# Kernel tuning notes

Measured on AMD Instinct MI355X. Metric: run time of the kernel, lower is better.

## Reference

```python
import jax, jax.numpy as jnp
import numpy as np

CH = 64
CF = CH // 8  # f/g projection channels


def setup_inputs() -> dict:
    key = jax.random.key(0)
    k1, k2, k3, k4, k5 = jax.random.split(key, 5)
    x = jax.random.normal(k1, (8, 64, 64, CH), dtype=jnp.float32)
    kernel_f = 0.02 * jax.random.normal(k2, (1, 1, CH, CF), dtype=jnp.float32)
    kernel_g = 0.02 * jax.random.normal(k3, (1, 1, CH, CF), dtype=jnp.float32)
    kernel_h = 0.02 * jax.random.normal(k4, (1, 1, CH, CH), dtype=jnp.float32)
    gamma = 0.02 * jax.random.normal(k5, (1,), dtype=jnp.float32)
    return {"x": x, "kernel_f": kernel_f, "kernel_g": kernel_g,
            "kernel_h": kernel_h, "gamma": gamma}


def reference(x, kernel_f, kernel_g, kernel_h, gamma):
    B, H, W, C = x.shape
    N = H * W
    xf = x.reshape(B, N, C)  # flatten spatial; 1x1 conv == matmul over channels
    f = jnp.einsum('bnc,cd->bnd', xf, kernel_f[0, 0])  # [B,N,CF]
    g = jnp.einsum('bnc,cd->bnd', xf, kernel_g[0, 0])  # [B,N,CF]
    h = jnp.einsum('bnc,cd->bnd', xf, kernel_h[0, 0])  # [B,N,C]
    s = jnp.einsum('bnd,bmd->bnm', g, f)  # g @ f^T, [B,N,N]
    beta = jax.nn.softmax(s, axis=-1)
    o = jnp.einsum('bnm,bmc->bnc', beta, h)  # [B,N,C]
    out = gamma * o.reshape(B, H, W, C) + x
    return out
```

## Files before the change

kernel.cpp:

```cpp
#include <hip/hip_runtime.h>
#include <hip/hip_bf16.h>

typedef __attribute__((ext_vector_type(4)))  float f32x4;
typedef __attribute__((ext_vector_type(16))) float f32x16;
typedef __attribute__((ext_vector_type(8)))  short bf16x8;

#define LOG2E 1.44269504088896340736f

#if __has_builtin(__builtin_amdgcn_exp2f)
static __device__ __forceinline__ float exp2_native(float x) {
  return __builtin_amdgcn_exp2f(x);
}
#else
extern "C" __device__ float __ocml_native_exp2_f32(float);
static __device__ __forceinline__ float exp2_native(float x) {
  return __ocml_native_exp2_f32(x);
}
#endif

static __device__ __forceinline__ unsigned int pack_trunc_f(float a, float b) {
  return __builtin_amdgcn_perm(__float_as_uint(b), __float_as_uint(a), 0x07060302);
}

typedef const __attribute__((address_space(1))) unsigned int gu32;
typedef __attribute__((address_space(3))) unsigned int lu32;
static __device__ __forceinline__ void gload_lds16(const void* g, void* l) {
  __builtin_amdgcn_global_load_lds((gu32*)g, (lu32*)l, 16, 0, 0);
}

__global__ __launch_bounds__(256) void proj_kernel(
    const float* __restrict__ x, const float* __restrict__ kf,
    const float* __restrict__ kg, const float* __restrict__ kh,
    unsigned short* __restrict__ f_b, unsigned short* __restrict__ g_b,
    unsigned short* __restrict__ h_p)
{
  __shared__ unsigned short Kt[80*72];
  const int t = threadIdx.x, blk = blockIdx.x;

  #pragma unroll
  for (int r = 0; r < 20; ++r) {
    int idx = r*256 + t;
    int o = idx >> 6, c = idx & 63;
    float v = (o < 8) ? kf[c*8 + o]
            : (o < 16) ? kg[c*8 + (o-8)] * LOG2E
            : kh[c*64 + (o-16)];
    Kt[o*72 + c] = (unsigned short)(__float_as_uint(v) >> 16);
  }
  __syncthreads();

  const int w = t >> 6, lane = t & 63, l15 = lane & 15, quad = lane >> 4;
  const int Rbase = blk*64 + w*16;
  const int R = Rbase + l15;

  bf16x8 af[2];
  #pragma unroll
  for (int kk = 0; kk < 2; ++kk) {
    const float* xp = x + (long)R*64 + kk*32 + quad*8;
    float4 v0 = *(const float4*)xp;
    float4 v1 = *(const float4*)(xp + 4);
    union { unsigned int u[4]; bf16x8 v; } p;
    p.u[0] = pack_trunc_f(v0.x, v0.y);
    p.u[1] = pack_trunc_f(v0.z, v0.w);
    p.u[2] = pack_trunc_f(v1.x, v1.y);
    p.u[3] = pack_trunc_f(v1.z, v1.w);
    af[kk] = p.v;
  }

  f32x4 acc[5];
  #pragma unroll
  for (int nt = 0; nt < 5; ++nt) { f32x4 z = {}; acc[nt] = z; }

  #pragma unroll
  for (int nt = 0; nt < 5; ++nt)
    #pragma unroll
    for (int kk = 0; kk < 2; ++kk) {
      bf16x8 bfv = *(const bf16x8*)&Kt[(nt*16 + l15)*72 + kk*32 + quad*8];
      acc[nt] = __builtin_amdgcn_mfma_f32_16x16x32_bf16(af[kk], bfv, acc[nt], 0, 0, 0);
    }

  const int bt = Rbase >> 12;
  const int kt = (Rbase >> 7) & 31;
  const int base = ((blk & 1) << 6) + (w << 4);
  const int pi = base + ((quad & 1) << 3) + (((quad >> 1) & 1) << 2);

  #pragma unroll
  for (int rr = 0; rr < 4; ++rr) {
    const int nq = (Rbase + quad*4 + rr) & 4095;
    unsigned short v = (unsigned short)(__float_as_uint(acc[0][rr]) >> 16);
    if (l15 < 8) f_b[((long)bt*4096 + nq)*8 + l15] = v;
    else         g_b[((long)bt*4096 + nq)*8 + (l15 - 8)] = v;
  }
  #pragma unroll
  for (int nt = 1; nt < 5; ++nt) {
    const int c = (nt - 1)*16 + l15;
    uint2 v;
    v.x = pack_trunc_f(acc[nt][0], acc[nt][1]);
    v.y = pack_trunc_f(acc[nt][2], acc[nt][3]);
    *(uint2*)(h_p + ((long)(bt*32 + kt)*64 + c)*136 + pi) = v;
  }
}

__global__ __launch_bounds__(256, 4) void attn_kernel(
    const unsigned short* __restrict__ f_b, const unsigned short* __restrict__ g_b,
    const unsigned short* __restrict__ h_p, unsigned short* __restrict__ po,
    float* __restrict__ pl)
{
  __shared__ unsigned short bufs[2][9728];

  const int t = threadIdx.x;
  const int w = t >> 6, lane = t & 63, l31 = lane & 31, a = lane >> 5;
  const int qb = blockIdx.x, b = blockIdx.y, sp = blockIdx.z;
  const int q0w = qb*128 + w*32;

  bf16x8 gfv;
  {
    bf16x8 gv = *(const bf16x8*)(g_b + ((long)b*4096 + q0w + l31)*8);
    bf16x8 z = {};
    gfv = (a == 0) ? gv : z;
  }

  f32x16 oacc[2];
  { f32x16 z = {}; oacc[0] = z; oacc[1] = z; }
  float l_run = 0.f;

  const char* hp_b = (const char*)h_p + (long)b*32*17408;
  const char* fb_b = (const char*)f_b + (long)b*4096*16;

  auto stage = [&](int bi, int kt) {
    const char* hsrc = hp_b + (long)kt*17408;
    const char* fsrc = fb_b + (long)kt*2048;
    char* dst = (char*)&bufs[bi][0];
    #pragma unroll
    for (int i = 0; i < 5; ++i) {
      const int off = i*4096 + w*1024;
      if (off < 19456) {
        const char* src = (off < 17408) ? (hsrc + off) : (fsrc + (off - 17408));
        gload_lds16(src + lane*16, dst + off);
      }
    }
  };

  stage(0, sp*8);

  for (int ktl = 0; ktl < 8; ++ktl) {
    __syncthreads();
    if (ktl < 7) stage((ktl + 1) & 1, sp*8 + ktl + 1);

    const unsigned short* hts = &bufs[ktl & 1][0];
    const unsigned short* fts = &bufs[ktl & 1][8704];

    #pragma unroll
    for (int mt = 0; mt < 4; ++mt) {
      bf16x8 afv = *(const bf16x8*)&fts[(mt*32 + l31)*8];
      f32x16 zz = {};
      f32x16 sc = __builtin_amdgcn_mfma_f32_32x32x16_bf16(afv, gfv, zz, 0, 0, 0);

      #pragma unroll
      for (int half = 0; half < 2; ++half) {
        const int s = mt*2 + half;
        bf16x8 bh0 = *(const bf16x8*)&hts[(l31)*136      + s*16 + a*8];
        bf16x8 bh1 = *(const bf16x8*)&hts[(32 + l31)*136 + s*16 + a*8];
        union { unsigned int u[4]; bf16x8 v; } ap;
        #pragma unroll
        for (int j = 0; j < 4; ++j) {
          float ea = exp2_native(sc[half*8 + 2*j]);
          float eb = exp2_native(sc[half*8 + 2*j + 1]);
          l_run += ea;
          l_run += eb;
          ap.u[j] = pack_trunc_f(ea, eb);
        }
        oacc[0] = __builtin_amdgcn_mfma_f32_32x32x16_bf16(ap.v, bh0, oacc[0], 0, 0, 0);
        oacc[1] = __builtin_amdgcn_mfma_f32_32x32x16_bf16(ap.v, bh1, oacc[1], 0, 0, 0);
      }
    }
  }

  const long sb = (long)sp*8 + b;
  float l = l_run + __shfl_xor(l_run, 32);
  if (lane < 32) pl[(sb << 12) + q0w + l31] = l;
  unsigned short* pob = po + ((sb << 12) + q0w)*64;
  #pragma unroll
  for (int nt = 0; nt < 2; ++nt)
    #pragma unroll
    for (int r = 0; r < 16; ++r) {
      const int q = (r & 3) + 8*(r >> 2) + 4*a;
      pob[(long)q*64 + nt*32 + l31] =
          (unsigned short)(__float_as_uint(oacc[nt][r]) >> 16);
    }
}

__global__ __launch_bounds__(256) void combine_kernel(
    const float* __restrict__ x, const unsigned short* __restrict__ po,
    const float* __restrict__ pl, const float* __restrict__ gamma_p,
    float* __restrict__ out)
{
  const long tid = (long)blockIdx.x*256 + threadIdx.x;
  const long bn = tid >> 3;
  const int c0 = (int)(tid & 7)*8;

  float l = 0.f;
  float o[8];
  #pragma unroll
  for (int i = 0; i < 8; ++i) o[i] = 0.f;
  #pragma unroll
  for (int s = 0; s < 4; ++s) {
    l += pl[(long)s*32768 + bn];
    uint4 v = *(const uint4*)(po + ((long)s*32768 + bn)*64 + c0);
    const unsigned short* pv = (const unsigned short*)&v;
    #pragma unroll
    for (int i = 0; i < 8; ++i)
      o[i] += __uint_as_float((unsigned int)pv[i] << 16);
  }
  const float scale = gamma_p[0] / l;
  const float* xp = x + bn*64 + c0;
  float4 x0 = *(const float4*)xp;
  float4 x1 = *(const float4*)(xp + 4);
  float4 r0, r1;
  r0.x = fmaf(scale, o[0], x0.x);
  r0.y = fmaf(scale, o[1], x0.y);
  r0.z = fmaf(scale, o[2], x0.z);
  r0.w = fmaf(scale, o[3], x0.w);
  r1.x = fmaf(scale, o[4], x1.x);
  r1.y = fmaf(scale, o[5], x1.y);
  r1.z = fmaf(scale, o[6], x1.z);
  r1.w = fmaf(scale, o[7], x1.w);
  float* op = out + bn*64 + c0;
  *(float4*)op = r0;
  *(float4*)(op + 4) = r1;
}

extern "C" void kernel_launch(void* const* d_in, const int* in_sizes, int n_in,
                              void* d_out, int out_size, void* d_ws, size_t ws_size,
                              hipStream_t stream) {
  const float* x  = (const float*)d_in[0];
  const float* kf = (const float*)d_in[1];
  const float* kg = (const float*)d_in[2];
  const float* kh = (const float*)d_in[3];
  const float* gamma = (const float*)d_in[4];
  float* out = (float*)d_out;

  char* ws = (char*)d_ws;
  unsigned short* h_p = (unsigned short*)ws;
  unsigned short* f_b = (unsigned short*)(ws + 4456448);
  unsigned short* g_b = (unsigned short*)(ws + 4980736);
  unsigned short* po  = (unsigned short*)(ws + 5505024);
  float*          pl  = (float*)(ws + 22282240);

  proj_kernel<<<512, 256, 0, stream>>>(x, kf, kg, kh, f_b, g_b, h_p);
  attn_kernel<<<dim3(32, 8, 4), 256, 0, stream>>>(f_b, g_b, h_p, po, pl);
  combine_kernel<<<1024, 256, 0, stream>>>(x, po, pl, gamma, out);
}
```

Before: 104.3 us.

## Fuse split-K combine into attention kernel via last-block atomic counter

Drops the separate combine kernel. Each attention block now bumps a per-(query-tile, batch) atomic counter after writing its partial outputs. The last of the four split blocks to arrive reduces the partials and writes gamma*o + x. The counters are zeroed by block 0 of the projection kernel. This saves one kernel launch and its tail. The cost is a threadfence, an atomic per block and extra register pressure for the 32-element accumulator on the finishing blocks.

Result: slower. 238.2 us (+128.3%).

```diff
diff --git a/kernel.cpp b/kernel.cpp
--- a/kernel.cpp
+++ b/kernel.cpp
@@ -32,10 +32,12 @@
     const float* __restrict__ x, const float* __restrict__ kf,
     const float* __restrict__ kg, const float* __restrict__ kh,
     unsigned short* __restrict__ f_b, unsigned short* __restrict__ g_b,
-    unsigned short* __restrict__ h_p)
+    unsigned short* __restrict__ h_p, int* __restrict__ cnt)
 {
   __shared__ unsigned short Kt[80*72];
   const int t = threadIdx.x, blk = blockIdx.x;
+
+  if (blk == 0) cnt[t] = 0;
 
   #pragma unroll
   for (int r = 0; r < 20; ++r) {
@@ -103,9 +105,12 @@
 __global__ __launch_bounds__(256, 4) void attn_kernel(
     const unsigned short* __restrict__ f_b, const unsigned short* __restrict__ g_b,
     const unsigned short* __restrict__ h_p, unsigned short* __restrict__ po,
-    float* __restrict__ pl)
+    float* __restrict__ pl, int* __restrict__ cnt,
+    const float* __restrict__ x, const float* __restrict__ gamma_p,
+    float* __restrict__ out)
 {
   __shared__ unsigned short bufs[2][9728];
+  __shared__ int sflag;
 
   const int t = threadIdx.x;
   const int w = t >> 6, lane = t & 63, l31 = lane & 31, a = lane >> 5;
@@ -187,46 +192,49 @@
       pob[(long)q*64 + nt*32 + l31] =
           (unsigned short)(__float_as_uint(oacc[nt][r]) >> 16);
     }
-}
-
-__global__ __launch_bounds__(256) void combine_kernel(
-    const float* __restrict__ x, const unsigned short* __restrict__ po,
-    const float* __restrict__ pl, const float* __restrict__ gamma_p,
-    float* __restrict__ out)
-{
-  const long tid = (long)blockIdx.x*256 + threadIdx.x;
-  const long bn = tid >> 3;
-  const int c0 = (int)(tid & 7)*8;
-
-  float l = 0.f;
-  float o[8];
-  #pragma unroll
-  for (int i = 0; i < 8; ++i) o[i] = 0.f;
+
+  __threadfence();
+  if (t == 0) {
+    int old = atomicAdd(&cnt[qb*8 + b], 1);
+    sflag = (old == 3);
+  }
+  __syncthreads();
+  if (!sflag) return;
+  __threadfence();
+
+  const int q = qb*128 + (t >> 1);
+  const int c0 = (t & 1) * 32;
+  float lsum = 0.f;
+  float o[32];
+  #pragma unroll
+  for (int i = 0; i < 32; ++i) o[i] = 0.f;
   #pragma unroll
   for (int s = 0; s < 4; ++s) {
-    l += pl[(long)s*32768 + bn];
-    uint4 v = *(const uint4*)(po + ((long)s*32768 + bn)*64 + c0);
-    const unsigned short* pv = (const unsigned short*)&v;
-    #pragma unroll
-    for (int i = 0; i < 8; ++i)
-      o[i] += __uint_as_float((unsigned int)pv[i] << 16);
-  }
-  const float scale = gamma_p[0] / l;
-  const float* xp = x + bn*64 + c0;
-  float4 x0 = *(const float4*)xp;
-  float4 x1 = *(const float4*)(xp + 4);
-  float4 r0, r1;
-  r0.x = fmaf(scale, o[0], x0.x);
-  r0.y = fmaf(scale, o[1], x0.y);
-  r0.z = fmaf(scale, o[2], x0.z);
-  r0.w = fmaf(scale, o[3], x0.w);
-  r1.x = fmaf(scale, o[4], x1.x);
-  r1.y = fmaf(scale, o[5], x1.y);
-  r1.z = fmaf(scale, o[6], x1.z);
-  r1.w = fmaf(scale, o[7], x1.w);
-  float* op = out + bn*64 + c0;
-  *(float4*)op = r0;
-  *(float4*)(op + 4) = r1;
+    const long sbb = (long)s*8 + b;
+    lsum += pl[(sbb << 12) + q];
+    const unsigned short* ps = po + ((sbb << 12) + q)*64 + c0;
+    #pragma unroll
+    for (int v4 = 0; v4 < 4; ++v4) {
+      uint4 v = *(const uint4*)(ps + v4*8);
+      const unsigned short* pv = (const unsigned short*)&v;
+      #pragma unroll
+      for (int i = 0; i < 8; ++i)
+        o[v4*8 + i] += __uint_as_float((unsigned int)pv[i] << 16);
+    }
+  }
+  const float scale = gamma_p[0] / lsum;
+  const float* xp = x + ((long)b*4096 + q)*64 + c0;
+  float* op = out + ((long)b*4096 + q)*64 + c0;
+  #pragma unroll
+  for (int v4 = 0; v4 < 8; ++v4) {
+    float4 xv = *(const float4*)(xp + v4*4);
+    float4 r;
+    r.x = fmaf(scale, o[v4*4 + 0], xv.x);
+    r.y = fmaf(scale, o[v4*4 + 1], xv.y);
+    r.z = fmaf(scale, o[v4*4 + 2], xv.z);
+    r.w = fmaf(scale, o[v4*4 + 3], xv.w);
+    *(float4*)(op + v4*4) = r;
+  }
 }
 
 extern "C" void kernel_launch(void* const* d_in, const int* in_sizes, int n_in,
@@ -245,8 +253,9 @@
   unsigned short* g_b = (unsigned short*)(ws + 4980736);
   unsigned short* po  = (unsigned short*)(ws + 5505024);
   float*          pl  = (float*)(ws + 22282240);
-
-  proj_kernel<<<512, 256, 0, stream>>>(x, kf, kg, kh, f_b, g_b, h_p);
-  attn_kernel<<<dim3(32, 8, 4), 256, 0, stream>>>(f_b, g_b, h_p, po, pl);
-  combine_kernel<<<1024, 256, 0, stream>>>(x, po, pl, gamma, out);
-}
+  int*            cnt = (int*)(ws + 22806528);
+
+  proj_kernel<<<512, 256, 0, stream>>>(x, kf, kg, kh, f_b, g_b, h_p, cnt);
+  attn_kernel<<<dim3(32, 8, 4), 256, 0, stream>>>(f_b, g_b, h_p, po, pl, cnt,
+                                                  x, gamma, out);
+}
```

## Drop split-K over keys and fuse the combine epilogue into attention

Applied to the files above, without the earlier changes.

Each attention block now iterates over all key tiles instead of a quarter of them. It applies the gamma/l scaling and residual add directly, which removes the partial-output buffers and the separate combine kernel. This saves a launch and the write and read of the bf16 partial results. The trade-off is a grid four times smaller with longer blocks, which lowers per-CU parallelism and latency hiding.

Result: slower. 116.1 us (+11.3%).

```diff
diff --git a/kernel.cpp b/kernel.cpp
--- a/kernel.cpp
+++ b/kernel.cpp
@@ -100,16 +100,17 @@
   }
 }
 
-__global__ __launch_bounds__(256, 4) void attn_kernel(
+__global__ __launch_bounds__(256) void attn_kernel(
     const unsigned short* __restrict__ f_b, const unsigned short* __restrict__ g_b,
-    const unsigned short* __restrict__ h_p, unsigned short* __restrict__ po,
-    float* __restrict__ pl)
+    const unsigned short* __restrict__ h_p,
+    const float* __restrict__ x, const float* __restrict__ gamma_p,
+    float* __restrict__ out)
 {
   __shared__ unsigned short bufs[2][9728];
 
   const int t = threadIdx.x;
   const int w = t >> 6, lane = t & 63, l31 = lane & 31, a = lane >> 5;
-  const int qb = blockIdx.x, b = blockIdx.y, sp = blockIdx.z;
+  const int qb = blockIdx.x, b = blockIdx.y;
   const int q0w = qb*128 + w*32;
 
   bf16x8 gfv;
@@ -140,11 +141,11 @@
     }
   };
 
-  stage(0, sp*8);
-
-  for (int ktl = 0; ktl < 8; ++ktl) {
+  stage(0, 0);
+
+  for (int ktl = 0; ktl < 32; ++ktl) {
     __syncthreads();
-    if (ktl < 7) stage((ktl + 1) & 1, sp*8 + ktl + 1);
+    if (ktl < 31) stage((ktl + 1) & 1, ktl + 1);
 
     const unsigned short* hts = &bufs[ktl & 1][0];
     const unsigned short* fts = &bufs[ktl & 1][8704];
@@ -175,58 +176,22 @@
     }
   }
 
-  const long sb = (long)sp*8 + b;
-  float l = l_run + __shfl_xor(l_run, 32);
-  if (lane < 32) pl[(sb << 12) + q0w + l31] = l;
-  unsigned short* pob = po + ((sb << 12) + q0w)*64;
-  #pragma unroll
-  for (int nt = 0; nt < 2; ++nt)
-    #pragma unroll
-    for (int r = 0; r < 16; ++r) {
-      const int q = (r & 3) + 8*(r >> 2) + 4*a;
-      pob[(long)q*64 + nt*32 + l31] =
-          (unsigned short)(__float_as_uint(oacc[nt][r]) >> 16);
-    }
-}
-
-__global__ __launch_bounds__(256) void combine_kernel(
-    const float* __restrict__ x, const unsigned short* __restrict__ po,
-    const float* __restrict__ pl, const float* __restrict__ gamma_p,
-    float* __restrict__ out)
-{
-  const long tid = (long)blockIdx.x*256 + threadIdx.x;
-  const long bn = tid >> 3;
-  const int c0 = (int)(tid & 7)*8;
-
-  float l = 0.f;
-  float o[8];
-  #pragma unroll
-  for (int i = 0; i < 8; ++i) o[i] = 0.f;
-  #pragma unroll
-  for (int s = 0; s < 4; ++s) {
-    l += pl[(long)s*32768 + bn];
-    uint4 v = *(const uint4*)(po + ((long)s*32768 + bn)*64 + c0);
-    const unsigned short* pv = (const unsigned short*)&v;
-    #pragma unroll
-    for (int i = 0; i < 8; ++i)
-      o[i] += __uint_as_float((unsigned int)pv[i] << 16);
-  }
-  const float scale = gamma_p[0] / l;
-  const float* xp = x + bn*64 + c0;
-  float4 x0 = *(const float4*)xp;
-  float4 x1 = *(const float4*)(xp + 4);
-  float4 r0, r1;
-  r0.x = fmaf(scale, o[0], x0.x);
-  r0.y = fmaf(scale, o[1], x0.y);
-  r0.z = fmaf(scale, o[2], x0.z);
-  r0.w = fmaf(scale, o[3], x0.w);
-  r1.x = fmaf(scale, o[4], x1.x);
-  r1.y = fmaf(scale, o[5], x1.y);
-  r1.z = fmaf(scale, o[6], x1.z);
-  r1.w = fmaf(scale, o[7], x1.w);
-  float* op = out + bn*64 + c0;
-  *(float4*)op = r0;
-  *(float4*)(op + 4) = r1;
+  const float l = l_run + __shfl_xor(l_run, 32);
+  const float gamma = gamma_p[0];
+  const float* xb = x + ((long)b*4096 + q0w)*64;
+  float* ob = out + ((long)b*4096 + q0w)*64;
+
+  #pragma unroll
+  for (int r = 0; r < 16; ++r) {
+    const int q = (r & 3) + 8*(r >> 2) + 4*a;
+    const float lq = __shfl(l, q);
+    const float s = gamma / lq;
+    #pragma unroll
+    for (int nt = 0; nt < 2; ++nt) {
+      const long idx = (long)q*64 + nt*32 + l31;
+      ob[idx] = fmaf(s, oacc[nt][r], xb[idx]);
+    }
+  }
 }
 
 extern "C" void kernel_launch(void* const* d_in, const int* in_sizes, int n_in,
@@ -243,10 +208,7 @@
   unsigned short* h_p = (unsigned short*)ws;
   unsigned short* f_b = (unsigned short*)(ws + 4456448);
   unsigned short* g_b = (unsigned short*)(ws + 4980736);
-  unsigned short* po  = (unsigned short*)(ws + 5505024);
-  float*          pl  = (float*)(ws + 22282240);
 
   proj_kernel<<<512, 256, 0, stream>>>(x, kf, kg, kh, f_b, g_b, h_p);
-  attn_kernel<<<dim3(32, 8, 4), 256, 0, stream>>>(f_b, g_b, h_p, po, pl);
-  combine_kernel<<<1024, 256, 0, stream>>>(x, po, pl, gamma, out);
-}
+  attn_kernel<<<dim3(32, 8), 256, 0, stream>>>(f_b, g_b, h_p, x, gamma, out);
+}
```
